# Performance work log

Hardware: AMD Instinct MI355X
Metric: run time of the kernel (lower is better)

Reference implementation:

```python
import jax, jax.numpy as jnp
import numpy as np

B = 131072

def _lin(x, w, b):
    return x @ w.T + b

def setup_inputs() -> dict:
    key = jax.random.key(0)
    ks = jax.random.split(key, 32)
    def rn(k, shape, scale=0.05):
        return jax.random.normal(k, shape, dtype=jnp.float32) * scale
    inp = {
        "x": rn(ks[0], (B, 256), 1.0),
        "w": rn(ks[1], (B, 36), 1.0),
        "h0": rn(ks[2], (B, 32), 1.0),
        "c0": rn(ks[3], (B, 32), 1.0),
        "fc1_w": rn(ks[4], (128, 256)), "fc1_b": rn(ks[5], (128,)),
        "fc1a_w": rn(ks[6], (128, 164)), "fc1a_b": rn(ks[7], (128,)),
        "fc1b_w": rn(ks[8], (128, 128)), "fc1b_b": rn(ks[9], (128,)),
        "w_game": rn(ks[10], (1, 12), 1.0),
        "fc1c_w": rn(ks[11], (64, 140)), "fc1c_b": rn(ks[12], (64,)),
        "fc2_w": rn(ks[13], (32, 64)), "fc2_b": rn(ks[14], (32,)),
        "fc3_w": rn(ks[15], (32, 32)), "fc3_b": rn(ks[16], (32,)),
        "w_ih": rn(ks[17], (128, 32)), "w_hh": rn(ks[18], (128, 32)),
        "b_ih": rn(ks[19], (128,)), "b_hh": rn(ks[20], (128,)),
        "fc4_w": rn(ks[21], (32, 32)), "fc4_b": rn(ks[22], (32,)),
        "fc5_w": rn(ks[23], (1, 32)), "fc5_b": rn(ks[24], (1,)),
    }
    return inp

def reference(x, w, h0, c0, fc1_w, fc1_b, fc1a_w, fc1a_b, fc1b_w, fc1b_b,
              w_game, fc1c_w, fc1c_b, fc2_w, fc2_b, fc3_w, fc3_b,
              w_ih, w_hh, b_ih, b_hh, fc4_w, fc4_b, fc5_w, fc5_b):
    b = x.shape[0]
    h = jax.nn.relu(_lin(x, fc1_w, fc1_b))                      # [B,128]
    h = jnp.concatenate([h, w], axis=-1)                        # [B,164]
    h = jax.nn.relu(_lin(h, fc1a_w, fc1a_b))                    # [B,128]
    h = jax.nn.relu(_lin(h, fc1b_w, fc1b_b))                    # [B,128]
    wg = jnp.broadcast_to(w_game.reshape(1, 12), (b, 12))
    h = jnp.concatenate([h, wg], axis=-1)                       # [B,140]
    h = jax.nn.relu(_lin(h, fc1c_w, fc1c_b))                    # [B,64]
    h = jax.nn.relu(_lin(h, fc2_w, fc2_b))                      # [B,32]
    h = jax.nn.relu(_lin(h, fc3_w, fc3_b))                      # [B,32]
    # LSTMCell step (torch gate order: input, forget, cell, output)
    gates = _lin(h, w_ih, b_ih) + _lin(h0, w_hh, b_hh)          # [B,128]
    i_g, f_g, g_g, o_g = jnp.split(gates, 4, axis=-1)
    c_new = jax.nn.sigmoid(f_g) * c0 + jax.nn.sigmoid(i_g) * jnp.tanh(g_g)
    h_new = jax.nn.sigmoid(o_g) * jnp.tanh(c_new)               # [B,32]
    out = jax.nn.relu(_lin(h_new, fc4_w, fc4_b))                # [B,32]
    out = _lin(out, fc5_w, fc5_b)                               # [B,1]
    return jax.nn.sigmoid(out)
```

## Files before the change

### kernel.cpp

```cpp
#include <hip/hip_runtime.h>
#include <hip/hip_bf16.h>


typedef __bf16 bf16x8 __attribute__((ext_vector_type(8)));
typedef float  f32x4  __attribute__((ext_vector_type(4)));
typedef int    i32x4  __attribute__((ext_vector_type(4)));

#define MFMA16(A, B, C) __builtin_amdgcn_mfma_f32_16x16x32_bf16((A), (B), (C), 0, 0, 0)

#define WOFF_FC1    0
#define WOFF_FC1A_H 32768
#define WOFF_FC1B   49152
#define WOFF_FC1C   65536
#define LDS_ELEMS   73728
#define WOFF_FC1A_W 73728
#define WOFF_FC2    81920
#define WOFF_FC3    83968
#define WOFF_WIH    84992
#define WOFF_WHH    89088
#define WOFF_FC4    93184
#define WTOT        94208
#define BOFF_FC1  0
#define BOFF_FC1A 128
#define BOFF_FC1B 256
#define BOFF_FC1C 384
#define BOFF_FC2  448
#define BOFF_FC3  480
#define BOFF_LSTM 512
#define BOFF_FC4  640
#define BTOT      672

__device__ __forceinline__ void conv_frag(int rel, const float* __restrict__ src,
                                          __bf16* __restrict__ dst,
                                          int ns, int Krow, int kbase, int klim, int perm) {
    int j    = rel & 7;
    int lane = (rel >> 3) & 63;
    int fs   = rel >> 9;
    int s    = fs % ns;
    int t    = fs / ns;
    int gq   = lane >> 4;
    int n    = 16 * t + (lane & 15);
    int k    = perm ? (16 * (2 * s + (j >> 2)) + 4 * gq + (j & 3))
                    : (32 * s + 8 * gq + j);
    float v  = (k < klim) ? src[n * Krow + kbase + k] : 0.f;
    dst[rel] = (__bf16)v;
}

__global__ void prep_kernel(const float* __restrict__ fc1w,  const float* __restrict__ fc1b,
                            const float* __restrict__ fc1aw, const float* __restrict__ fc1ab,
                            const float* __restrict__ fc1bw, const float* __restrict__ fc1bb,
                            const float* __restrict__ wgame, const float* __restrict__ fc1cw,
                            const float* __restrict__ fc1cb, const float* __restrict__ fc2w,
                            const float* __restrict__ fc2b,  const float* __restrict__ fc3w,
                            const float* __restrict__ fc3b,  const float* __restrict__ wih,
                            const float* __restrict__ whh,   const float* __restrict__ bih,
                            const float* __restrict__ bhh,   const float* __restrict__ fc4w,
                            const float* __restrict__ fc4b,
                            __bf16* __restrict__ wsw, float* __restrict__ wsb) {
    int idx = blockIdx.x * 256 + threadIdx.x;
    if (idx < WTOT) {
        if      (idx < WOFF_FC1A_H) conv_frag(idx - WOFF_FC1,    fc1w,  wsw + WOFF_FC1,    8, 256,   0, 256, 0);
        else if (idx < WOFF_FC1B)   conv_frag(idx - WOFF_FC1A_H, fc1aw, wsw + WOFF_FC1A_H, 4, 164,   0, 128, 1);
        else if (idx < WOFF_FC1C)   conv_frag(idx - WOFF_FC1B,   fc1bw, wsw + WOFF_FC1B,   4, 128,   0, 128, 1);
        else if (idx < WOFF_FC1A_W) conv_frag(idx - WOFF_FC1C,   fc1cw, wsw + WOFF_FC1C,   4, 140,   0, 128, 1);
        else if (idx < WOFF_FC2)    conv_frag(idx - WOFF_FC1A_W, fc1aw, wsw + WOFF_FC1A_W, 2, 164, 128,  36, 0);
        else if (idx < WOFF_FC3)    conv_frag(idx - WOFF_FC2,    fc2w,  wsw + WOFF_FC2,    2,  64,   0,  64, 1);
        else if (idx < WOFF_WIH)    conv_frag(idx - WOFF_FC3,    fc3w,  wsw + WOFF_FC3,    1,  32,   0,  32, 1);
        else if (idx < WOFF_WHH)    conv_frag(idx - WOFF_WIH,    wih,   wsw + WOFF_WIH,    1,  32,   0,  32, 1);
        else if (idx < WOFF_FC4)    conv_frag(idx - WOFF_WHH,    whh,   wsw + WOFF_WHH,    1,  32,   0,  32, 0);
        else                        conv_frag(idx - WOFF_FC4,    fc4w,  wsw + WOFF_FC4,    1,  32,   0,  32, 1);
    } else if (idx < WTOT + BTOT) {
        int bi = idx - WTOT;
        float v;
        if      (bi < 128) v = fc1b[bi];
        else if (bi < 256) v = fc1ab[bi - 128];
        else if (bi < 384) v = fc1bb[bi - 256];
        else if (bi < 448) {
            int n = bi - 384;
            v = fc1cb[n];
            for (int q = 0; q < 12; ++q) v += fc1cw[n * 140 + 128 + q] * wgame[q];
        }
        else if (bi < 480) v = fc2b[bi - 448];
        else if (bi < 512) v = fc3b[bi - 480];
        else if (bi < 640) { int n = bi - 512; v = bih[n] + bhh[n]; }
        else               v = fc4b[bi - 640];
        wsb[bi] = v;
    }
}

__device__ __forceinline__ bf16x8 ld8f(const float* __restrict__ p) {
    f32x4 a = *(const f32x4*)p;
    f32x4 b = *(const f32x4*)(p + 4);
    bf16x8 r;
    r[0] = (__bf16)a[0]; r[1] = (__bf16)a[1]; r[2] = (__bf16)a[2]; r[3] = (__bf16)a[3];
    r[4] = (__bf16)b[0]; r[5] = (__bf16)b[1]; r[6] = (__bf16)b[2]; r[7] = (__bf16)b[3];
    return r;
}

__device__ __forceinline__ bf16x8 ld4f_masked(const float* __restrict__ p, bool on) {
    f32x4 v = {0.f, 0.f, 0.f, 0.f};
    if (on) v = *(const f32x4*)p;
    bf16x8 r;
    r[0] = (__bf16)v[0]; r[1] = (__bf16)v[1]; r[2] = (__bf16)v[2]; r[3] = (__bf16)v[3];
    r[4] = (__bf16)0.f;  r[5] = (__bf16)0.f;  r[6] = (__bf16)0.f;  r[7] = (__bf16)0.f;
    return r;
}

__device__ __forceinline__ bf16x8 packrelu(const f32x4* a, int s) {
    bf16x8 r;
#pragma unroll
    for (int j = 0; j < 8; ++j) {
        float v = a[2 * s + (j >> 2)][j & 3];
        r[j] = (__bf16)fmaxf(v, 0.f);
    }
    return r;
}

__device__ __forceinline__ float sigm(float v)  { return 1.f / (1.f + __expf(-v)); }
__device__ __forceinline__ float tanh_(float v) { return 1.f - 2.f / (1.f + __expf(2.f * v)); }

__global__ __launch_bounds__(512, 2) void fused_mlp_lstm(
        const float* __restrict__ x,  const float* __restrict__ w,
        const float* __restrict__ h0, const float* __restrict__ c0,
        const float* __restrict__ fc5w, const float* __restrict__ fc5b,
        const __bf16* __restrict__ wsw, const float* __restrict__ wsb,
        float* __restrict__ out) {
    __shared__ __align__(16) __bf16 slds[LDS_ELEMS];

    const int tid     = threadIdx.x;
    const int lane    = tid & 63;
    const int wv      = blockIdx.x * 8 + (tid >> 6);
    const int gq      = lane >> 4;
    const int mr      = lane & 15;
    const int rowbase = wv * 32;
    const int row0    = rowbase + mr;
    const int row1    = rowbase + 16 + mr;

    {
        const i32x4* gs = (const i32x4*)wsw;
        i32x4*       sd = (i32x4*)slds;
#pragma unroll
        for (int i = 0; i < 18; ++i) sd[i * 512 + tid] = gs[i * 512 + tid];
    }

    bf16x8 xf[2][8];
#pragma unroll
    for (int s = 0; s < 8; ++s) {
        xf[0][s] = ld8f(x + row0 * 256 + 32 * s + 8 * gq);
        xf[1][s] = ld8f(x + row1 * 256 + 32 * s + 8 * gq);
    }
    bf16x8 wxa0 = ld8f(w + row0 * 36 + 8 * gq);
    bf16x8 wxb0 = ld8f(w + row1 * 36 + 8 * gq);
    bf16x8 wxa1 = ld4f_masked(w + row0 * 36 + 32, gq == 0);
    bf16x8 wxb1 = ld4f_masked(w + row1 * 36 + 32, gq == 0);

    __syncthreads();

    const bf16x8* Wfc1  = (const bf16x8*)(slds + WOFF_FC1);
    const bf16x8* Wf1aH = (const bf16x8*)(slds + WOFF_FC1A_H);
    const bf16x8* Wfc1b = (const bf16x8*)(slds + WOFF_FC1B);
    const bf16x8* Wfc1c = (const bf16x8*)(slds + WOFF_FC1C);
    const bf16x8* Wf1aW = (const bf16x8*)(wsw + WOFF_FC1A_W);
    const bf16x8* Wfc2  = (const bf16x8*)(wsw + WOFF_FC2);
    const bf16x8* Wfc3  = (const bf16x8*)(wsw + WOFF_FC3);
    const bf16x8* Wwih  = (const bf16x8*)(wsw + WOFF_WIH);
    const bf16x8* Wwhh  = (const bf16x8*)(wsw + WOFF_WHH);
    const bf16x8* Wfc4  = (const bf16x8*)(wsw + WOFF_FC4);

    f32x4 acc1[2][8];
#pragma unroll
    for (int t = 0; t < 8; ++t) {
        f32x4 bv = *(const f32x4*)(wsb + BOFF_FC1 + 16 * t + 4 * gq);
        acc1[0][t] = bv; acc1[1][t] = bv;
    }
#pragma unroll
    for (int s = 0; s < 8; ++s) {
#pragma unroll
        for (int t = 0; t < 8; ++t) {
            bf16x8 wf = Wfc1[(t * 8 + s) * 64 + lane];
            acc1[0][t] = MFMA16(wf, xf[0][s], acc1[0][t]);
            acc1[1][t] = MFMA16(wf, xf[1][s], acc1[1][t]);
        }
    }
    bf16x8 h0fa = ld8f(h0 + row0 * 32 + 8 * gq);
    bf16x8 h0fb = ld8f(h0 + row1 * 32 + 8 * gq);

    bf16x8 h1f[2][4];
#pragma unroll
    for (int s = 0; s < 4; ++s) { h1f[0][s] = packrelu(acc1[0], s); h1f[1][s] = packrelu(acc1[1], s); }

    f32x4 acc2[2][8];
#pragma unroll
    for (int t = 0; t < 8; ++t) {
        f32x4 bv = *(const f32x4*)(wsb + BOFF_FC1A + 16 * t + 4 * gq);
        acc2[0][t] = bv; acc2[1][t] = bv;
    }
#pragma unroll
    for (int s = 0; s < 4; ++s) {
#pragma unroll
        for (int t = 0; t < 8; ++t) {
            bf16x8 wf = Wf1aH[(t * 4 + s) * 64 + lane];
            acc2[0][t] = MFMA16(wf, h1f[0][s], acc2[0][t]);
            acc2[1][t] = MFMA16(wf, h1f[1][s], acc2[1][t]);
        }
    }
#pragma unroll
    for (int t = 0; t < 8; ++t) {
        bf16x8 wf0 = Wf1aW[(t * 2 + 0) * 64 + lane];
        bf16x8 wf1 = Wf1aW[(t * 2 + 1) * 64 + lane];
        acc2[0][t] = MFMA16(wf0, wxa0, acc2[0][t]);
        acc2[1][t] = MFMA16(wf0, wxb0, acc2[1][t]);
        acc2[0][t] = MFMA16(wf1, wxa1, acc2[0][t]);
        acc2[1][t] = MFMA16(wf1, wxb1, acc2[1][t]);
    }
    f32x4 c0r[2][2];
#pragma unroll
    for (int t2 = 0; t2 < 2; ++t2) {
        c0r[0][t2] = *(const f32x4*)(c0 + row0 * 32 + 16 * t2 + 4 * gq);
        c0r[1][t2] = *(const f32x4*)(c0 + row1 * 32 + 16 * t2 + 4 * gq);
    }

    bf16x8 h2f[2][4];
#pragma unroll
    for (int s = 0; s < 4; ++s) { h2f[0][s] = packrelu(acc2[0], s); h2f[1][s] = packrelu(acc2[1], s); }

    f32x4 acc3[2][8];
#pragma unroll
    for (int t = 0; t < 8; ++t) {
        f32x4 bv = *(const f32x4*)(wsb + BOFF_FC1B + 16 * t + 4 * gq);
        acc3[0][t] = bv; acc3[1][t] = bv;
    }
#pragma unroll
    for (int s = 0; s < 4; ++s) {
#pragma unroll
        for (int t = 0; t < 8; ++t) {
            bf16x8 wf = Wfc1b[(t * 4 + s) * 64 + lane];
            acc3[0][t] = MFMA16(wf, h2f[0][s], acc3[0][t]);
            acc3[1][t] = MFMA16(wf, h2f[1][s], acc3[1][t]);
        }
    }
    bf16x8 h3f[2][4];
#pragma unroll
    for (int s = 0; s < 4; ++s) { h3f[0][s] = packrelu(acc3[0], s); h3f[1][s] = packrelu(acc3[1], s); }

    f32x4 acc4[2][4];
#pragma unroll
    for (int t = 0; t < 4; ++t) {
        f32x4 bv = *(const f32x4*)(wsb + BOFF_FC1C + 16 * t + 4 * gq);
        acc4[0][t] = bv; acc4[1][t] = bv;
    }
#pragma unroll
    for (int s = 0; s < 4; ++s) {
#pragma unroll
        for (int t = 0; t < 4; ++t) {
            bf16x8 wf = Wfc1c[(t * 4 + s) * 64 + lane];
            acc4[0][t] = MFMA16(wf, h3f[0][s], acc4[0][t]);
            acc4[1][t] = MFMA16(wf, h3f[1][s], acc4[1][t]);
        }
    }
    bf16x8 h4f[2][2];
#pragma unroll
    for (int s = 0; s < 2; ++s) { h4f[0][s] = packrelu(acc4[0], s); h4f[1][s] = packrelu(acc4[1], s); }

    f32x4 acc5[2][2];
#pragma unroll
    for (int t = 0; t < 2; ++t) {
        f32x4 bv = *(const f32x4*)(wsb + BOFF_FC2 + 16 * t + 4 * gq);
        acc5[0][t] = bv; acc5[1][t] = bv;
    }
#pragma unroll
    for (int s = 0; s < 2; ++s) {
#pragma unroll
        for (int t = 0; t < 2; ++t) {
            bf16x8 wf = Wfc2[(t * 2 + s) * 64 + lane];
            acc5[0][t] = MFMA16(wf, h4f[0][s], acc5[0][t]);
            acc5[1][t] = MFMA16(wf, h4f[1][s], acc5[1][t]);
        }
    }
    bf16x8 h5f[2] = { packrelu(acc5[0], 0), packrelu(acc5[1], 0) };

    f32x4 acc6[2][2];
#pragma unroll
    for (int t = 0; t < 2; ++t) {
        f32x4 bv = *(const f32x4*)(wsb + BOFF_FC3 + 16 * t + 4 * gq);
        acc6[0][t] = bv; acc6[1][t] = bv;
    }
#pragma unroll
    for (int t = 0; t < 2; ++t) {
        bf16x8 wf = Wfc3[t * 64 + lane];
        acc6[0][t] = MFMA16(wf, h5f[0], acc6[0][t]);
        acc6[1][t] = MFMA16(wf, h5f[1], acc6[1][t]);
    }
    bf16x8 h6f[2] = { packrelu(acc6[0], 0), packrelu(acc6[1], 0) };

    f32x4 accg[2][8];
#pragma unroll
    for (int t = 0; t < 8; ++t) {
        f32x4 bv = *(const f32x4*)(wsb + BOFF_LSTM + 16 * t + 4 * gq);
        accg[0][t] = bv; accg[1][t] = bv;
    }
#pragma unroll
    for (int t = 0; t < 8; ++t) {
        bf16x8 wf = Wwih[t * 64 + lane];
        accg[0][t] = MFMA16(wf, h6f[0], accg[0][t]);
        accg[1][t] = MFMA16(wf, h6f[1], accg[1][t]);
    }
#pragma unroll
    for (int t = 0; t < 8; ++t) {
        bf16x8 wf = Wwhh[t * 64 + lane];
        accg[0][t] = MFMA16(wf, h0fa, accg[0][t]);
        accg[1][t] = MFMA16(wf, h0fb, accg[1][t]);
    }
    float hn[2][8];
#pragma unroll
    for (int m = 0; m < 2; ++m) {
#pragma unroll
        for (int t2 = 0; t2 < 2; ++t2) {
            f32x4 cc = c0r[m][t2];
#pragma unroll
            for (int r = 0; r < 4; ++r) {
                float ig = accg[m][t2][r];
                float fg = accg[m][2 + t2][r];
                float gg = accg[m][4 + t2][r];
                float og = accg[m][6 + t2][r];
                float cn = sigm(fg) * cc[r] + sigm(ig) * tanh_(gg);
                hn[m][t2 * 4 + r] = sigm(og) * tanh_(cn);
            }
        }
    }
    bf16x8 hnf[2];
#pragma unroll
    for (int m = 0; m < 2; ++m)
#pragma unroll
        for (int j = 0; j < 8; ++j) hnf[m][j] = (__bf16)hn[m][j];

    f32x4 acco[2][2];
#pragma unroll
    for (int t = 0; t < 2; ++t) {
        f32x4 bv = *(const f32x4*)(wsb + BOFF_FC4 + 16 * t + 4 * gq);
        acco[0][t] = bv; acco[1][t] = bv;
    }
#pragma unroll
    for (int t = 0; t < 2; ++t) {
        bf16x8 wf = Wfc4[t * 64 + lane];
        acco[0][t] = MFMA16(wf, hnf[0], acco[0][t]);
        acco[1][t] = MFMA16(wf, hnf[1], acco[1][t]);
    }

    f32x4 w5a = *(const f32x4*)(fc5w + 4 * gq);
    f32x4 w5b = *(const f32x4*)(fc5w + 16 + 4 * gq);
    float b5  = fc5b[0];
    float res[2];
#pragma unroll
    for (int m = 0; m < 2; ++m) {
        float p = 0.f;
#pragma unroll
        for (int r = 0; r < 4; ++r) {
            p += fmaxf(acco[m][0][r], 0.f) * w5a[r];
            p += fmaxf(acco[m][1][r], 0.f) * w5b[r];
        }
        p += __shfl_xor(p, 16);
        p += __shfl_xor(p, 32);
        res[m] = sigm(p + b5);
    }
    if (lane < 16) {
        out[rowbase + lane]      = res[0];
        out[rowbase + 16 + lane] = res[1];
    }
}

extern "C" void kernel_launch(void* const* d_in, const int* in_sizes, int n_in,
                              void* d_out, int out_size, void* d_ws, size_t ws_size,
                              hipStream_t stream) {
    const float* x     = (const float*)d_in[0];
    const float* w     = (const float*)d_in[1];
    const float* h0    = (const float*)d_in[2];
    const float* c0    = (const float*)d_in[3];
    const float* fc1w  = (const float*)d_in[4];
    const float* fc1b  = (const float*)d_in[5];
    const float* fc1aw = (const float*)d_in[6];
    const float* fc1ab = (const float*)d_in[7];
    const float* fc1bw = (const float*)d_in[8];
    const float* fc1bb = (const float*)d_in[9];
    const float* wgame = (const float*)d_in[10];
    const float* fc1cw = (const float*)d_in[11];
    const float* fc1cb = (const float*)d_in[12];
    const float* fc2w  = (const float*)d_in[13];
    const float* fc2b  = (const float*)d_in[14];
    const float* fc3w  = (const float*)d_in[15];
    const float* fc3b  = (const float*)d_in[16];
    const float* wih   = (const float*)d_in[17];
    const float* whh   = (const float*)d_in[18];
    const float* bih   = (const float*)d_in[19];
    const float* bhh   = (const float*)d_in[20];
    const float* fc4w  = (const float*)d_in[21];
    const float* fc4b  = (const float*)d_in[22];
    const float* fc5w  = (const float*)d_in[23];
    const float* fc5b  = (const float*)d_in[24];

    __bf16* wsw = (__bf16*)d_ws;
    float*  wsb = (float*)((char*)d_ws + WTOT * sizeof(__bf16));
    (void)ws_size; (void)n_in; (void)out_size;

    const int Btot = in_sizes[0] / 256;

    prep_kernel<<<(WTOT + BTOT + 255) / 256, 256, 0, stream>>>(
        fc1w, fc1b, fc1aw, fc1ab, fc1bw, fc1bb, wgame, fc1cw, fc1cb,
        fc2w, fc2b, fc3w, fc3b, wih, whh, bih, bhh, fc4w, fc4b, wsw, wsb);

    fused_mlp_lstm<<<Btot / 256, 512, 0, stream>>>(
        x, w, h0, c0, fc5w, fc5b, wsw, wsb, (float*)d_out);
}
```

Before: 64.32 us.

## Convert LDS-resident weights in the main kernel and double block size

The main kernel now reads the fp32 fc1/fc1a/fc1b/fc1c weights and converts them to bf16 MFMA fragments directly into LDS, instead of copying a pre-swizzled bf16 buffer written by the prep kernel. The prep kernel shrinks to the small global-resident weights and the biases. Blocks grow from 512 to 1024 threads, so each block's LDS fill is shared by 16 waves instead of 8. The h0 loads are also hoisted ahead of the barrier. In exchange, each block does redundant fp32 loads and conversion work, __launch_bounds__(1024,4) may constrain registers in this MFMA-heavy kernel, and halving the grid reduces the number of blocks.

```diff
diff --git a/kernel.cpp b/kernel.cpp
--- a/kernel.cpp
+++ b/kernel.cpp
@@ -4,7 +4,6 @@
 
 typedef __bf16 bf16x8 __attribute__((ext_vector_type(8)));
 typedef float  f32x4  __attribute__((ext_vector_type(4)));
-typedef int    i32x4  __attribute__((ext_vector_type(4)));
 
 #define MFMA16(A, B, C) __builtin_amdgcn_mfma_f32_16x16x32_bf16((A), (B), (C), 0, 0, 0)
 
@@ -46,9 +45,33 @@
     dst[rel] = (__bf16)v;
 }
 
-__global__ void prep_kernel(const float* __restrict__ fc1w,  const float* __restrict__ fc1b,
-                            const float* __restrict__ fc1aw, const float* __restrict__ fc1ab,
-                            const float* __restrict__ fc1bw, const float* __restrict__ fc1bb,
+__device__ __forceinline__ bf16x8 conv8(int rel8, const float* __restrict__ src,
+                                        int ns, int Krow, int perm) {
+    int lane = (rel8 >> 3) & 63;
+    int fs   = rel8 >> 9;
+    int s    = fs % ns;
+    int t    = fs / ns;
+    int gq   = lane >> 4;
+    int n    = 16 * t + (lane & 15);
+    const float* rowp = src + n * Krow;
+    f32x4 a, b;
+    if (perm) {
+        int k0 = 32 * s + 4 * gq;
+        a = *(const f32x4*)(rowp + k0);
+        b = *(const f32x4*)(rowp + k0 + 16);
+    } else {
+        int k0 = 32 * s + 8 * gq;
+        a = *(const f32x4*)(rowp + k0);
+        b = *(const f32x4*)(rowp + k0 + 4);
+    }
+    bf16x8 r;
+    r[0] = (__bf16)a[0]; r[1] = (__bf16)a[1]; r[2] = (__bf16)a[2]; r[3] = (__bf16)a[3];
+    r[4] = (__bf16)b[0]; r[5] = (__bf16)b[1]; r[6] = (__bf16)b[2]; r[7] = (__bf16)b[3];
+    return r;
+}
+
+__global__ void prep_kernel(const float* __restrict__ fc1aw, const float* __restrict__ fc1b,
+                            const float* __restrict__ fc1ab, const float* __restrict__ fc1bb,
                             const float* __restrict__ wgame, const float* __restrict__ fc1cw,
                             const float* __restrict__ fc1cb, const float* __restrict__ fc2w,
                             const float* __restrict__ fc2b,  const float* __restrict__ fc3w,
@@ -57,18 +80,14 @@
                             const float* __restrict__ bhh,   const float* __restrict__ fc4w,
                             const float* __restrict__ fc4b,
                             __bf16* __restrict__ wsw, float* __restrict__ wsb) {
-    int idx = blockIdx.x * 256 + threadIdx.x;
+    int idx = blockIdx.x * 256 + threadIdx.x + LDS_ELEMS;
     if (idx < WTOT) {
-        if      (idx < WOFF_FC1A_H) conv_frag(idx - WOFF_FC1,    fc1w,  wsw + WOFF_FC1,    8, 256,   0, 256, 0);
-        else if (idx < WOFF_FC1B)   conv_frag(idx - WOFF_FC1A_H, fc1aw, wsw + WOFF_FC1A_H, 4, 164,   0, 128, 1);
-        else if (idx < WOFF_FC1C)   conv_frag(idx - WOFF_FC1B,   fc1bw, wsw + WOFF_FC1B,   4, 128,   0, 128, 1);
-        else if (idx < WOFF_FC1A_W) conv_frag(idx - WOFF_FC1C,   fc1cw, wsw + WOFF_FC1C,   4, 140,   0, 128, 1);
-        else if (idx < WOFF_FC2)    conv_frag(idx - WOFF_FC1A_W, fc1aw, wsw + WOFF_FC1A_W, 2, 164, 128,  36, 0);
-        else if (idx < WOFF_FC3)    conv_frag(idx - WOFF_FC2,    fc2w,  wsw + WOFF_FC2,    2,  64,   0,  64, 1);
-        else if (idx < WOFF_WIH)    conv_frag(idx - WOFF_FC3,    fc3w,  wsw + WOFF_FC3,    1,  32,   0,  32, 1);
-        else if (idx < WOFF_WHH)    conv_frag(idx - WOFF_WIH,    wih,   wsw + WOFF_WIH,    1,  32,   0,  32, 1);
-        else if (idx < WOFF_FC4)    conv_frag(idx - WOFF_WHH,    whh,   wsw + WOFF_WHH,    1,  32,   0,  32, 0);
-        else                        conv_frag(idx - WOFF_FC4,    fc4w,  wsw + WOFF_FC4,    1,  32,   0,  32, 1);
+        if      (idx < WOFF_FC2)  conv_frag(idx - WOFF_FC1A_W, fc1aw, wsw + WOFF_FC1A_W, 2, 164, 128, 36, 0);
+        else if (idx < WOFF_FC3)  conv_frag(idx - WOFF_FC2,    fc2w,  wsw + WOFF_FC2,    2,  64,   0, 64, 1);
+        else if (idx < WOFF_WIH)  conv_frag(idx - WOFF_FC3,    fc3w,  wsw + WOFF_FC3,    1,  32,   0, 32, 1);
+        else if (idx < WOFF_WHH)  conv_frag(idx - WOFF_WIH,    wih,   wsw + WOFF_WIH,    1,  32,   0, 32, 1);
+        else if (idx < WOFF_FC4)  conv_frag(idx - WOFF_WHH,    whh,   wsw + WOFF_WHH,    1,  32,   0, 32, 0);
+        else                      conv_frag(idx - WOFF_FC4,    fc4w,  wsw + WOFF_FC4,    1,  32,   0, 32, 1);
     } else if (idx < WTOT + BTOT) {
         int bi = idx - WTOT;
         float v;
@@ -119,28 +138,34 @@
 __device__ __forceinline__ float sigm(float v)  { return 1.f / (1.f + __expf(-v)); }
 __device__ __forceinline__ float tanh_(float v) { return 1.f - 2.f / (1.f + __expf(2.f * v)); }
 
-__global__ __launch_bounds__(512, 2) void fused_mlp_lstm(
+__global__ __launch_bounds__(1024, 4) void fused_mlp_lstm(
         const float* __restrict__ x,  const float* __restrict__ w,
         const float* __restrict__ h0, const float* __restrict__ c0,
         const float* __restrict__ fc5w, const float* __restrict__ fc5b,
+        const float* __restrict__ fc1w, const float* __restrict__ fc1aw,
+        const float* __restrict__ fc1bw, const float* __restrict__ fc1cw,
         const __bf16* __restrict__ wsw, const float* __restrict__ wsb,
         float* __restrict__ out) {
     __shared__ __align__(16) __bf16 slds[LDS_ELEMS];
 
     const int tid     = threadIdx.x;
     const int lane    = tid & 63;
-    const int wv      = blockIdx.x * 8 + (tid >> 6);
+    const int wv      = blockIdx.x * 16 + (tid >> 6);
     const int gq      = lane >> 4;
     const int mr      = lane & 15;
     const int rowbase = wv * 32;
     const int row0    = rowbase + mr;
     const int row1    = rowbase + 16 + mr;
 
-    {
-        const i32x4* gs = (const i32x4*)wsw;
-        i32x4*       sd = (i32x4*)slds;
-#pragma unroll
-        for (int i = 0; i < 18; ++i) sd[i * 512 + tid] = gs[i * 512 + tid];
+#pragma unroll 3
+    for (int i = 0; i < 9; ++i) {
+        int rel8 = (i * 1024 + tid) * 8;
+        bf16x8 v;
+        if      (rel8 < WOFF_FC1A_H) v = conv8(rel8 - WOFF_FC1,    fc1w,  8, 256, 0);
+        else if (rel8 < WOFF_FC1B)   v = conv8(rel8 - WOFF_FC1A_H, fc1aw, 4, 164, 1);
+        else if (rel8 < WOFF_FC1C)   v = conv8(rel8 - WOFF_FC1B,   fc1bw, 4, 128, 1);
+        else                         v = conv8(rel8 - WOFF_FC1C,   fc1cw, 4, 140, 1);
+        *(bf16x8*)(slds + rel8) = v;
     }
 
     bf16x8 xf[2][8];
@@ -153,6 +178,8 @@
     bf16x8 wxb0 = ld8f(w + row1 * 36 + 8 * gq);
     bf16x8 wxa1 = ld4f_masked(w + row0 * 36 + 32, gq == 0);
     bf16x8 wxb1 = ld4f_masked(w + row1 * 36 + 32, gq == 0);
+    bf16x8 h0fa = ld8f(h0 + row0 * 32 + 8 * gq);
+    bf16x8 h0fb = ld8f(h0 + row1 * 32 + 8 * gq);
 
     __syncthreads();
 
@@ -182,9 +209,6 @@
             acc1[1][t] = MFMA16(wf, xf[1][s], acc1[1][t]);
         }
     }
-    bf16x8 h0fa = ld8f(h0 + row0 * 32 + 8 * gq);
-    bf16x8 h0fb = ld8f(h0 + row1 * 32 + 8 * gq);
-
     bf16x8 h1f[2][4];
 #pragma unroll
     for (int s = 0; s < 4; ++s) { h1f[0][s] = packrelu(acc1[0], s); h1f[1][s] = packrelu(acc1[1], s); }
@@ -404,10 +428,11 @@
 
     const int Btot = in_sizes[0] / 256;
 
-    prep_kernel<<<(WTOT + BTOT + 255) / 256, 256, 0, stream>>>(
-        fc1w, fc1b, fc1aw, fc1ab, fc1bw, fc1bb, wgame, fc1cw, fc1cb,
+    prep_kernel<<<((WTOT - LDS_ELEMS) + BTOT + 255) / 256, 256, 0, stream>>>(
+        fc1aw, fc1b, fc1ab, fc1bb, wgame, fc1cw, fc1cb,
         fc2w, fc2b, fc3w, fc3b, wih, whh, bih, bhh, fc4w, fc4b, wsw, wsb);
 
-    fused_mlp_lstm<<<Btot / 256, 512, 0, stream>>>(
-        x, w, h0, c0, fc5w, fc5b, wsw, wsb, (float*)d_out);
-}
+    fused_mlp_lstm<<<Btot / 512, 1024, 0, stream>>>(
+        x, w, h0, c0, fc5w, fc5b, fc1w, fc1aw, fc1bw, fc1cw,
+        wsw, wsb, (float*)d_out);
+}
```

Result: slower. 94.85 us (+47.5%).

## Read fc1 weights from global memory, shrink LDS, and raise occupancy

Applied to the files above, without the earlier changes.

fc1 weights now stay in global memory (L2-cached) and no longer go to LDS, which cuts shared memory per block from 144KB to 80KB. The x, w, h0 and c0 loads are moved next to where they are used, which shortens register live ranges. Launch bounds are raised to 4 blocks of 512 threads to get more waves per CU. The risks are that fc1 weight fetches from L2/global are slower than LDS reads, and that input-load latency is no longer overlapped with the LDS fill. LDS may still cap occupancy below the requested 4 blocks.

```diff
diff --git a/kernel.cpp b/kernel.cpp
--- a/kernel.cpp
+++ b/kernel.cpp
@@ -8,11 +8,11 @@
 
 #define MFMA16(A, B, C) __builtin_amdgcn_mfma_f32_16x16x32_bf16((A), (B), (C), 0, 0, 0)
 
-#define WOFF_FC1    0
-#define WOFF_FC1A_H 32768
-#define WOFF_FC1B   49152
-#define WOFF_FC1C   65536
-#define LDS_ELEMS   73728
+#define WOFF_FC1A_H 0
+#define WOFF_FC1B   16384
+#define WOFF_FC1C   32768
+#define LDS_ELEMS   40960
+#define WOFF_FC1    40960
 #define WOFF_FC1A_W 73728
 #define WOFF_FC2    81920
 #define WOFF_FC3    83968
@@ -59,10 +59,10 @@
                             __bf16* __restrict__ wsw, float* __restrict__ wsb) {
     int idx = blockIdx.x * 256 + threadIdx.x;
     if (idx < WTOT) {
-        if      (idx < WOFF_FC1A_H) conv_frag(idx - WOFF_FC1,    fc1w,  wsw + WOFF_FC1,    8, 256,   0, 256, 0);
-        else if (idx < WOFF_FC1B)   conv_frag(idx - WOFF_FC1A_H, fc1aw, wsw + WOFF_FC1A_H, 4, 164,   0, 128, 1);
+        if      (idx < WOFF_FC1B)   conv_frag(idx - WOFF_FC1A_H, fc1aw, wsw + WOFF_FC1A_H, 4, 164,   0, 128, 1);
         else if (idx < WOFF_FC1C)   conv_frag(idx - WOFF_FC1B,   fc1bw, wsw + WOFF_FC1B,   4, 128,   0, 128, 1);
-        else if (idx < WOFF_FC1A_W) conv_frag(idx - WOFF_FC1C,   fc1cw, wsw + WOFF_FC1C,   4, 140,   0, 128, 1);
+        else if (idx < WOFF_FC1)    conv_frag(idx - WOFF_FC1C,   fc1cw, wsw + WOFF_FC1C,   4, 140,   0, 128, 1);
+        else if (idx < WOFF_FC1A_W) conv_frag(idx - WOFF_FC1,    fc1w,  wsw + WOFF_FC1,    8, 256,   0, 256, 0);
         else if (idx < WOFF_FC2)    conv_frag(idx - WOFF_FC1A_W, fc1aw, wsw + WOFF_FC1A_W, 2, 164, 128,  36, 0);
         else if (idx < WOFF_FC3)    conv_frag(idx - WOFF_FC2,    fc2w,  wsw + WOFF_FC2,    2,  64,   0,  64, 1);
         else if (idx < WOFF_WIH)    conv_frag(idx - WOFF_FC3,    fc3w,  wsw + WOFF_FC3,    1,  32,   0,  32, 1);
@@ -119,7 +119,7 @@
 __device__ __forceinline__ float sigm(float v)  { return 1.f / (1.f + __expf(-v)); }
 __device__ __forceinline__ float tanh_(float v) { return 1.f - 2.f / (1.f + __expf(2.f * v)); }
 
-__global__ __launch_bounds__(512, 2) void fused_mlp_lstm(
+__global__ __launch_bounds__(512, 4) void fused_mlp_lstm(
         const float* __restrict__ x,  const float* __restrict__ w,
         const float* __restrict__ h0, const float* __restrict__ c0,
         const float* __restrict__ fc5w, const float* __restrict__ fc5b,
@@ -140,23 +140,10 @@
         const i32x4* gs = (const i32x4*)wsw;
         i32x4*       sd = (i32x4*)slds;
 #pragma unroll
-        for (int i = 0; i < 18; ++i) sd[i * 512 + tid] = gs[i * 512 + tid];
-    }
-
-    bf16x8 xf[2][8];
-#pragma unroll
-    for (int s = 0; s < 8; ++s) {
-        xf[0][s] = ld8f(x + row0 * 256 + 32 * s + 8 * gq);
-        xf[1][s] = ld8f(x + row1 * 256 + 32 * s + 8 * gq);
-    }
-    bf16x8 wxa0 = ld8f(w + row0 * 36 + 8 * gq);
-    bf16x8 wxb0 = ld8f(w + row1 * 36 + 8 * gq);
-    bf16x8 wxa1 = ld4f_masked(w + row0 * 36 + 32, gq == 0);
-    bf16x8 wxb1 = ld4f_masked(w + row1 * 36 + 32, gq == 0);
-
-    __syncthreads();
-
-    const bf16x8* Wfc1  = (const bf16x8*)(slds + WOFF_FC1);
+        for (int i = 0; i < 10; ++i) sd[i * 512 + tid] = gs[i * 512 + tid];
+    }
+
+    const bf16x8* Gfc1  = (const bf16x8*)(wsw + WOFF_FC1);
     const bf16x8* Wf1aH = (const bf16x8*)(slds + WOFF_FC1A_H);
     const bf16x8* Wfc1b = (const bf16x8*)(slds + WOFF_FC1B);
     const bf16x8* Wfc1c = (const bf16x8*)(slds + WOFF_FC1C);
@@ -175,15 +162,17 @@
     }
 #pragma unroll
     for (int s = 0; s < 8; ++s) {
+        bf16x8 xa = ld8f(x + row0 * 256 + 32 * s + 8 * gq);
+        bf16x8 xb = ld8f(x + row1 * 256 + 32 * s + 8 * gq);
 #pragma unroll
         for (int t = 0; t < 8; ++t) {
-            bf16x8 wf = Wfc1[(t * 8 + s) * 64 + lane];
-            acc1[0][t] = MFMA16(wf, xf[0][s], acc1[0][t]);
-            acc1[1][t] = MFMA16(wf, xf[1][s], acc1[1][t]);
-        }
-    }
-    bf16x8 h0fa = ld8f(h0 + row0 * 32 + 8 * gq);
-    bf16x8 h0fb = ld8f(h0 + row1 * 32 + 8 * gq);
+            bf16x8 wf = Gfc1[(t * 8 + s) * 64 + lane];
+            acc1[0][t] = MFMA16(wf, xa, acc1[0][t]);
+            acc1[1][t] = MFMA16(wf, xb, acc1[1][t]);
+        }
+    }
+
+    __syncthreads();
 
     bf16x8 h1f[2][4];
 #pragma unroll
@@ -204,22 +193,21 @@
             acc2[1][t] = MFMA16(wf, h1f[1][s], acc2[1][t]);
         }
     }
-#pragma unroll
-    for (int t = 0; t < 8; ++t) {
-        bf16x8 wf0 = Wf1aW[(t * 2 + 0) * 64 + lane];
-        bf16x8 wf1 = Wf1aW[(t * 2 + 1) * 64 + lane];
-        acc2[0][t] = MFMA16(wf0, wxa0, acc2[0][t]);
-        acc2[1][t] = MFMA16(wf0, wxb0, acc2[1][t]);
-        acc2[0][t] = MFMA16(wf1, wxa1, acc2[0][t]);
-        acc2[1][t] = MFMA16(wf1, wxb1, acc2[1][t]);
-    }
-    f32x4 c0r[2][2];
-#pragma unroll
-    for (int t2 = 0; t2 < 2; ++t2) {
-        c0r[0][t2] = *(const f32x4*)(c0 + row0 * 32 + 16 * t2 + 4 * gq);
-        c0r[1][t2] = *(const f32x4*)(c0 + row1 * 32 + 16 * t2 + 4 * gq);
-    }
-
+    {
+        bf16x8 wxa0 = ld8f(w + row0 * 36 + 8 * gq);
+        bf16x8 wxb0 = ld8f(w + row1 * 36 + 8 * gq);
+        bf16x8 wxa1 = ld4f_masked(w + row0 * 36 + 32, gq == 0);
+        bf16x8 wxb1 = ld4f_masked(w + row1 * 36 + 32, gq == 0);
+#pragma unroll
+        for (int t = 0; t < 8; ++t) {
+            bf16x8 wf0 = Wf1aW[(t * 2 + 0) * 64 + lane];
+            bf16x8 wf1 = Wf1aW[(t * 2 + 1) * 64 + lane];
+            acc2[0][t] = MFMA16(wf0, wxa0, acc2[0][t]);
+            acc2[1][t] = MFMA16(wf0, wxb0, acc2[1][t]);
+            acc2[0][t] = MFMA16(wf1, wxa1, acc2[0][t]);
+            acc2[1][t] = MFMA16(wf1, wxb1, acc2[1][t]);
+        }
+    }
     bf16x8 h2f[2][4];
 #pragma unroll
     for (int s = 0; s < 4; ++s) { h2f[0][s] = packrelu(acc2[0], s); h2f[1][s] = packrelu(acc2[1], s); }
@@ -305,18 +293,23 @@
         accg[0][t] = MFMA16(wf, h6f[0], accg[0][t]);
         accg[1][t] = MFMA16(wf, h6f[1], accg[1][t]);
     }
-#pragma unroll
-    for (int t = 0; t < 8; ++t) {
-        bf16x8 wf = Wwhh[t * 64 + lane];
-        accg[0][t] = MFMA16(wf, h0fa, accg[0][t]);
-        accg[1][t] = MFMA16(wf, h0fb, accg[1][t]);
+    {
+        bf16x8 h0fa = ld8f(h0 + row0 * 32 + 8 * gq);
+        bf16x8 h0fb = ld8f(h0 + row1 * 32 + 8 * gq);
+#pragma unroll
+        for (int t = 0; t < 8; ++t) {
+            bf16x8 wf = Wwhh[t * 64 + lane];
+            accg[0][t] = MFMA16(wf, h0fa, accg[0][t]);
+            accg[1][t] = MFMA16(wf, h0fb, accg[1][t]);
+        }
     }
     float hn[2][8];
 #pragma unroll
     for (int m = 0; m < 2; ++m) {
+        const int row = (m == 0) ? row0 : row1;
 #pragma unroll
         for (int t2 = 0; t2 < 2; ++t2) {
-            f32x4 cc = c0r[m][t2];
+            f32x4 cc = *(const f32x4*)(c0 + row * 32 + 16 * t2 + 4 * gq);
 #pragma unroll
             for (int r = 0; r < 4; ++r) {
                 float ig = accg[m][t2][r];
```

Result: slower. 68.21 us (+6.1%).

## Double block size and restructure layers to cut register pressure

Applied to the files above, without the earlier changes.

Moves to 1024-thread blocks that each stage the LDS weights once for 16 waves, halving the per-row weight-copy cost. The x and w inputs are now loaded just before use instead of all up front. The fc1a and fc1b layers are split into two output halves so fewer accumulators are live at once. Launch bounds ask for 4 waves per SIMD, which means a tighter VGPR budget and possible spills, and having fewer loads in flight may expose more memory latency.

```diff
diff --git a/kernel.cpp b/kernel.cpp
--- a/kernel.cpp
+++ b/kernel.cpp
@@ -119,7 +119,7 @@
 __device__ __forceinline__ float sigm(float v)  { return 1.f / (1.f + __expf(-v)); }
 __device__ __forceinline__ float tanh_(float v) { return 1.f - 2.f / (1.f + __expf(2.f * v)); }
 
-__global__ __launch_bounds__(512, 2) void fused_mlp_lstm(
+__global__ __launch_bounds__(1024, 4) void fused_mlp_lstm(
         const float* __restrict__ x,  const float* __restrict__ w,
         const float* __restrict__ h0, const float* __restrict__ c0,
         const float* __restrict__ fc5w, const float* __restrict__ fc5b,
@@ -129,7 +129,7 @@
 
     const int tid     = threadIdx.x;
     const int lane    = tid & 63;
-    const int wv      = blockIdx.x * 8 + (tid >> 6);
+    const int wv      = blockIdx.x * 16 + (tid >> 6);
     const int gq      = lane >> 4;
     const int mr      = lane & 15;
     const int rowbase = wv * 32;
@@ -140,20 +140,8 @@
         const i32x4* gs = (const i32x4*)wsw;
         i32x4*       sd = (i32x4*)slds;
 #pragma unroll
-        for (int i = 0; i < 18; ++i) sd[i * 512 + tid] = gs[i * 512 + tid];
-    }
-
-    bf16x8 xf[2][8];
-#pragma unroll
-    for (int s = 0; s < 8; ++s) {
-        xf[0][s] = ld8f(x + row0 * 256 + 32 * s + 8 * gq);
-        xf[1][s] = ld8f(x + row1 * 256 + 32 * s + 8 * gq);
-    }
-    bf16x8 wxa0 = ld8f(w + row0 * 36 + 8 * gq);
-    bf16x8 wxb0 = ld8f(w + row1 * 36 + 8 * gq);
-    bf16x8 wxa1 = ld4f_masked(w + row0 * 36 + 32, gq == 0);
-    bf16x8 wxb1 = ld4f_masked(w + row1 * 36 + 32, gq == 0);
-
+        for (int i = 0; i < 9; ++i) sd[i * 1024 + tid] = gs[i * 1024 + tid];
+    }
     __syncthreads();
 
     const bf16x8* Wfc1  = (const bf16x8*)(slds + WOFF_FC1);
@@ -167,52 +155,97 @@
     const bf16x8* Wwhh  = (const bf16x8*)(wsw + WOFF_WHH);
     const bf16x8* Wfc4  = (const bf16x8*)(wsw + WOFF_FC4);
 
-    f32x4 acc1[2][8];
-#pragma unroll
-    for (int t = 0; t < 8; ++t) {
-        f32x4 bv = *(const f32x4*)(wsb + BOFF_FC1 + 16 * t + 4 * gq);
-        acc1[0][t] = bv; acc1[1][t] = bv;
-    }
-#pragma unroll
-    for (int s = 0; s < 8; ++s) {
+    bf16x8 h1f[2][4];
+    {
+        f32x4 acc1[2][8];
 #pragma unroll
         for (int t = 0; t < 8; ++t) {
-            bf16x8 wf = Wfc1[(t * 8 + s) * 64 + lane];
-            acc1[0][t] = MFMA16(wf, xf[0][s], acc1[0][t]);
-            acc1[1][t] = MFMA16(wf, xf[1][s], acc1[1][t]);
-        }
-    }
+            f32x4 bv = *(const f32x4*)(wsb + BOFF_FC1 + 16 * t + 4 * gq);
+            acc1[0][t] = bv; acc1[1][t] = bv;
+        }
+#pragma unroll
+        for (int s = 0; s < 8; ++s) {
+            bf16x8 xa = ld8f(x + row0 * 256 + 32 * s + 8 * gq);
+            bf16x8 xb = ld8f(x + row1 * 256 + 32 * s + 8 * gq);
+#pragma unroll
+            for (int t = 0; t < 8; ++t) {
+                bf16x8 wf = Wfc1[(t * 8 + s) * 64 + lane];
+                acc1[0][t] = MFMA16(wf, xa, acc1[0][t]);
+                acc1[1][t] = MFMA16(wf, xb, acc1[1][t]);
+            }
+        }
+#pragma unroll
+        for (int s = 0; s < 4; ++s) { h1f[0][s] = packrelu(acc1[0], s); h1f[1][s] = packrelu(acc1[1], s); }
+    }
+
+    bf16x8 h2f[2][4];
+#pragma unroll
+    for (int th = 0; th < 2; ++th) {
+        f32x4 acc2[2][4];
+#pragma unroll
+        for (int tt = 0; tt < 4; ++tt) {
+            f32x4 bv = *(const f32x4*)(wsb + BOFF_FC1A + 16 * (4 * th + tt) + 4 * gq);
+            acc2[0][tt] = bv; acc2[1][tt] = bv;
+        }
+#pragma unroll
+        for (int s = 0; s < 4; ++s) {
+#pragma unroll
+            for (int tt = 0; tt < 4; ++tt) {
+                bf16x8 wf = Wf1aH[((4 * th + tt) * 4 + s) * 64 + lane];
+                acc2[0][tt] = MFMA16(wf, h1f[0][s], acc2[0][tt]);
+                acc2[1][tt] = MFMA16(wf, h1f[1][s], acc2[1][tt]);
+            }
+        }
+        {
+            bf16x8 wxa0 = ld8f(w + row0 * 36 + 8 * gq);
+            bf16x8 wxb0 = ld8f(w + row1 * 36 + 8 * gq);
+            bf16x8 wxa1 = ld4f_masked(w + row0 * 36 + 32, gq == 0);
+            bf16x8 wxb1 = ld4f_masked(w + row1 * 36 + 32, gq == 0);
+#pragma unroll
+            for (int tt = 0; tt < 4; ++tt) {
+                int t = 4 * th + tt;
+                bf16x8 wf0 = Wf1aW[(t * 2 + 0) * 64 + lane];
+                bf16x8 wf1 = Wf1aW[(t * 2 + 1) * 64 + lane];
+                acc2[0][tt] = MFMA16(wf0, wxa0, acc2[0][tt]);
+                acc2[1][tt] = MFMA16(wf0, wxb0, acc2[1][tt]);
+                acc2[0][tt] = MFMA16(wf1, wxa1, acc2[0][tt]);
+                acc2[1][tt] = MFMA16(wf1, wxb1, acc2[1][tt]);
+            }
+        }
+#pragma unroll
+        for (int sh = 0; sh < 2; ++sh) {
+            h2f[0][2 * th + sh] = packrelu(acc2[0], sh);
+            h2f[1][2 * th + sh] = packrelu(acc2[1], sh);
+        }
+    }
+
+    bf16x8 h3f[2][4];
+#pragma unroll
+    for (int th = 0; th < 2; ++th) {
+        f32x4 acc3[2][4];
+#pragma unroll
+        for (int tt = 0; tt < 4; ++tt) {
+            f32x4 bv = *(const f32x4*)(wsb + BOFF_FC1B + 16 * (4 * th + tt) + 4 * gq);
+            acc3[0][tt] = bv; acc3[1][tt] = bv;
+        }
+#pragma unroll
+        for (int s = 0; s < 4; ++s) {
+#pragma unroll
+            for (int tt = 0; tt < 4; ++tt) {
+                bf16x8 wf = Wfc1b[((4 * th + tt) * 4 + s) * 64 + lane];
+                acc3[0][tt] = MFMA16(wf, h2f[0][s], acc3[0][tt]);
+                acc3[1][tt] = MFMA16(wf, h2f[1][s], acc3[1][tt]);
+            }
+        }
+#pragma unroll
+        for (int sh = 0; sh < 2; ++sh) {
+            h3f[0][2 * th + sh] = packrelu(acc3[0], sh);
+            h3f[1][2 * th + sh] = packrelu(acc3[1], sh);
+        }
+    }
+
     bf16x8 h0fa = ld8f(h0 + row0 * 32 + 8 * gq);
     bf16x8 h0fb = ld8f(h0 + row1 * 32 + 8 * gq);
-
-    bf16x8 h1f[2][4];
-#pragma unroll
-    for (int s = 0; s < 4; ++s) { h1f[0][s] = packrelu(acc1[0], s); h1f[1][s] = packrelu(acc1[1], s); }
-
-    f32x4 acc2[2][8];
-#pragma unroll
-    for (int t = 0; t < 8; ++t) {
-        f32x4 bv = *(const f32x4*)(wsb + BOFF_FC1A + 16 * t + 4 * gq);
-        acc2[0][t] = bv; acc2[1][t] = bv;
-    }
-#pragma unroll
-    for (int s = 0; s < 4; ++s) {
-#pragma unroll
-        for (int t = 0; t < 8; ++t) {
-            bf16x8 wf = Wf1aH[(t * 4 + s) * 64 + lane];
-            acc2[0][t] = MFMA16(wf, h1f[0][s], acc2[0][t]);
-            acc2[1][t] = MFMA16(wf, h1f[1][s], acc2[1][t]);
-        }
-    }
-#pragma unroll
-    for (int t = 0; t < 8; ++t) {
-        bf16x8 wf0 = Wf1aW[(t * 2 + 0) * 64 + lane];
-        bf16x8 wf1 = Wf1aW[(t * 2 + 1) * 64 + lane];
-        acc2[0][t] = MFMA16(wf0, wxa0, acc2[0][t]);
-        acc2[1][t] = MFMA16(wf0, wxb0, acc2[1][t]);
-        acc2[0][t] = MFMA16(wf1, wxa1, acc2[0][t]);
-        acc2[1][t] = MFMA16(wf1, wxb1, acc2[1][t]);
-    }
     f32x4 c0r[2][2];
 #pragma unroll
     for (int t2 = 0; t2 < 2; ++t2) {
@@ -220,111 +253,98 @@
         c0r[1][t2] = *(const f32x4*)(c0 + row1 * 32 + 16 * t2 + 4 * gq);
     }
 
-    bf16x8 h2f[2][4];
-#pragma unroll
-    for (int s = 0; s < 4; ++s) { h2f[0][s] = packrelu(acc2[0], s); h2f[1][s] = packrelu(acc2[1], s); }
-
-    f32x4 acc3[2][8];
-#pragma unroll
-    for (int t = 0; t < 8; ++t) {
-        f32x4 bv = *(const f32x4*)(wsb + BOFF_FC1B + 16 * t + 4 * gq);
-        acc3[0][t] = bv; acc3[1][t] = bv;
-    }
-#pragma unroll
-    for (int s = 0; s < 4; ++s) {
+    bf16x8 h4f[2][2];
+    {
+        f32x4 acc4[2][4];
+#pragma unroll
+        for (int t = 0; t < 4; ++t) {
+            f32x4 bv = *(const f32x4*)(wsb + BOFF_FC1C + 16 * t + 4 * gq);
+            acc4[0][t] = bv; acc4[1][t] = bv;
+        }
+#pragma unroll
+        for (int s = 0; s < 4; ++s) {
+#pragma unroll
+            for (int t = 0; t < 4; ++t) {
+                bf16x8 wf = Wfc1c[(t * 4 + s) * 64 + lane];
+                acc4[0][t] = MFMA16(wf, h3f[0][s], acc4[0][t]);
+                acc4[1][t] = MFMA16(wf, h3f[1][s], acc4[1][t]);
+            }
+        }
+#pragma unroll
+        for (int s = 0; s < 2; ++s) { h4f[0][s] = packrelu(acc4[0], s); h4f[1][s] = packrelu(acc4[1], s); }
+    }
+
+    bf16x8 h5f[2];
+    {
+        f32x4 acc5[2][2];
+#pragma unroll
+        for (int t = 0; t < 2; ++t) {
+            f32x4 bv = *(const f32x4*)(wsb + BOFF_FC2 + 16 * t + 4 * gq);
+            acc5[0][t] = bv; acc5[1][t] = bv;
+        }
+#pragma unroll
+        for (int s = 0; s < 2; ++s) {
+#pragma unroll
+            for (int t = 0; t < 2; ++t) {
+                bf16x8 wf = Wfc2[(t * 2 + s) * 64 + lane];
+                acc5[0][t] = MFMA16(wf, h4f[0][s], acc5[0][t]);
+                acc5[1][t] = MFMA16(wf, h4f[1][s], acc5[1][t]);
+            }
+        }
+        h5f[0] = packrelu(acc5[0], 0); h5f[1] = packrelu(acc5[1], 0);
+    }
+
+    bf16x8 h6f[2];
+    {
+        f32x4 acc6[2][2];
+#pragma unroll
+        for (int t = 0; t < 2; ++t) {
+            f32x4 bv = *(const f32x4*)(wsb + BOFF_FC3 + 16 * t + 4 * gq);
+            acc6[0][t] = bv; acc6[1][t] = bv;
+        }
+#pragma unroll
+        for (int t = 0; t < 2; ++t) {
+            bf16x8 wf = Wfc3[t * 64 + lane];
+            acc6[0][t] = MFMA16(wf, h5f[0], acc6[0][t]);
+            acc6[1][t] = MFMA16(wf, h5f[1], acc6[1][t]);
+        }
+        h6f[0] = packrelu(acc6[0], 0); h6f[1] = packrelu(acc6[1], 0);
+    }
+
+    float hn[2][8];
+    {
+        f32x4 accg[2][8];
 #pragma unroll
         for (int t = 0; t < 8; ++t) {
-            bf16x8 wf = Wfc1b[(t * 4 + s) * 64 + lane];
-            acc3[0][t] = MFMA16(wf, h2f[0][s], acc3[0][t]);
-            acc3[1][t] = MFMA16(wf, h2f[1][s], acc3[1][t]);
-        }
-    }
-    bf16x8 h3f[2][4];
-#pragma unroll
-    for (int s = 0; s < 4; ++s) { h3f[0][s] = packrelu(acc3[0], s); h3f[1][s] = packrelu(acc3[1], s); }
-
-    f32x4 acc4[2][4];
-#pragma unroll
-    for (int t = 0; t < 4; ++t) {
-        f32x4 bv = *(const f32x4*)(wsb + BOFF_FC1C + 16 * t + 4 * gq);
-        acc4[0][t] = bv; acc4[1][t] = bv;
-    }
-#pragma unroll
-    for (int s = 0; s < 4; ++s) {
-#pragma unroll
-        for (int t = 0; t < 4; ++t) {
-            bf16x8 wf = Wfc1c[(t * 4 + s) * 64 + lane];
-            acc4[0][t] = MFMA16(wf, h3f[0][s], acc4[0][t]);
-            acc4[1][t] = MFMA16(wf, h3f[1][s], acc4[1][t]);
-        }
-    }
-    bf16x8 h4f[2][2];
-#pragma unroll
-    for (int s = 0; s < 2; ++s) { h4f[0][s] = packrelu(acc4[0], s); h4f[1][s] = packrelu(acc4[1], s); }
-
-    f32x4 acc5[2][2];
-#pragma unroll
-    for (int t = 0; t < 2; ++t) {
-        f32x4 bv = *(const f32x4*)(wsb + BOFF_FC2 + 16 * t + 4 * gq);
-        acc5[0][t] = bv; acc5[1][t] = bv;
-    }
-#pragma unroll
-    for (int s = 0; s < 2; ++s) {
-#pragma unroll
-        for (int t = 0; t < 2; ++t) {
-            bf16x8 wf = Wfc2[(t * 2 + s) * 64 + lane];
-            acc5[0][t] = MFMA16(wf, h4f[0][s], acc5[0][t]);
-            acc5[1][t] = MFMA16(wf, h4f[1][s], acc5[1][t]);
-        }
-    }
-    bf16x8 h5f[2] = { packrelu(acc5[0], 0), packrelu(acc5[1], 0) };
-
-    f32x4 acc6[2][2];
-#pragma unroll
-    for (int t = 0; t < 2; ++t) {
-        f32x4 bv = *(const f32x4*)(wsb + BOFF_FC3 + 16 * t + 4 * gq);
-        acc6[0][t] = bv; acc6[1][t] = bv;
-    }
-#pragma unroll
-    for (int t = 0; t < 2; ++t) {
-        bf16x8 wf = Wfc3[t * 64 + lane];
-        acc6[0][t] = MFMA16(wf, h5f[0], acc6[0][t]);
-        acc6[1][t] = MFMA16(wf, h5f[1], acc6[1][t]);
-    }
-    bf16x8 h6f[2] = { packrelu(acc6[0], 0), packrelu(acc6[1], 0) };
-
-    f32x4 accg[2][8];
-#pragma unroll
-    for (int t = 0; t < 8; ++t) {
-        f32x4 bv = *(const f32x4*)(wsb + BOFF_LSTM + 16 * t + 4 * gq);
-        accg[0][t] = bv; accg[1][t] = bv;
-    }
-#pragma unroll
-    for (int t = 0; t < 8; ++t) {
-        bf16x8 wf = Wwih[t * 64 + lane];
-        accg[0][t] = MFMA16(wf, h6f[0], accg[0][t]);
-        accg[1][t] = MFMA16(wf, h6f[1], accg[1][t]);
-    }
-#pragma unroll
-    for (int t = 0; t < 8; ++t) {
-        bf16x8 wf = Wwhh[t * 64 + lane];
-        accg[0][t] = MFMA16(wf, h0fa, accg[0][t]);
-        accg[1][t] = MFMA16(wf, h0fb, accg[1][t]);
-    }
-    float hn[2][8];
-#pragma unroll
-    for (int m = 0; m < 2; ++m) {
-#pragma unroll
-        for (int t2 = 0; t2 < 2; ++t2) {
-            f32x4 cc = c0r[m][t2];
-#pragma unroll
-            for (int r = 0; r < 4; ++r) {
-                float ig = accg[m][t2][r];
-                float fg = accg[m][2 + t2][r];
-                float gg = accg[m][4 + t2][r];
-                float og = accg[m][6 + t2][r];
-                float cn = sigm(fg) * cc[r] + sigm(ig) * tanh_(gg);
-                hn[m][t2 * 4 + r] = sigm(og) * tanh_(cn);
+            f32x4 bv = *(const f32x4*)(wsb + BOFF_LSTM + 16 * t + 4 * gq);
+            accg[0][t] = bv; accg[1][t] = bv;
+        }
+#pragma unroll
+        for (int t = 0; t < 8; ++t) {
+            bf16x8 wf = Wwih[t * 64 + lane];
+            accg[0][t] = MFMA16(wf, h6f[0], accg[0][t]);
+            accg[1][t] = MFMA16(wf, h6f[1], accg[1][t]);
+        }
+#pragma unroll
+        for (int t = 0; t < 8; ++t) {
+            bf16x8 wf = Wwhh[t * 64 + lane];
+            accg[0][t] = MFMA16(wf, h0fa, accg[0][t]);
+            accg[1][t] = MFMA16(wf, h0fb, accg[1][t]);
+        }
+#pragma unroll
+        for (int m = 0; m < 2; ++m) {
+#pragma unroll
+            for (int t2 = 0; t2 < 2; ++t2) {
+                f32x4 cc = c0r[m][t2];
+#pragma unroll
+                for (int r = 0; r < 4; ++r) {
+                    float ig = accg[m][t2][r];
+                    float fg = accg[m][2 + t2][r];
+                    float gg = accg[m][4 + t2][r];
+                    float og = accg[m][6 + t2][r];
+                    float cn = sigm(fg) * cc[r] + sigm(ig) * tanh_(gg);
+                    hn[m][t2 * 4 + r] = sigm(og) * tanh_(cn);
+                }
             }
         }
     }
@@ -408,6 +428,6 @@
         fc1w, fc1b, fc1aw, fc1ab, fc1bw, fc1bb, wgame, fc1cw, fc1cb,
         fc2w, fc2b, fc3w, fc3b, wih, whh, bih, bhh, fc4w, fc4b, wsw, wsb);
 
-    fused_mlp_lstm<<<Btot / 256, 512, 0, stream>>>(
+    fused_mlp_lstm<<<Btot / 512, 1024, 0, stream>>>(
         x, w, h0, c0, fc5w, fc5b, wsw, wsb, (float*)d_out);
 }
```

Measured after the change: 62.66 us. 2.6% less time.
